# Optimization experiments

Hardware: AMD Instinct MI355X
Metric: run time of the kernel (lower is better)

The kernel has to match this reference:

```python
import jax, jax.numpy as jnp
import numpy as np

N, E = 100_000, 1_000_000
D_IN, D_H, D_OUT = 64, 64, 16


def _lin_init(key, d_in, d_out):
    # torch.nn.Linear default: U(-1/sqrt(fan_in), 1/sqrt(fan_in))
    s = 1.0 / np.sqrt(d_in)
    kw, kb = jax.random.split(key)
    W = jax.random.uniform(kw, (d_in, d_out), jnp.float32, -s, s)
    b = jax.random.uniform(kb, (d_out,), jnp.float32, -s, s)
    return W, b


def setup_inputs() -> dict:
    key = jax.random.key(0)
    ks = jax.random.split(key, 8)
    x = jax.random.normal(ks[0], (N, D_IN), dtype=jnp.float32)
    edge_index = jax.random.randint(ks[1], (2, E), 0, N, dtype=jnp.int64)
    inp = {"x": x, "edge_index": edge_index}
    dims = [(D_IN, D_H), (D_H, D_H), (D_H, D_H), (D_H, D_H)]
    for i, (di, do) in enumerate(dims):
        W, b = _lin_init(ks[2 + i], di, do)
        inp[f"W{i}"] = W
        inp[f"b{i}"] = b
    W_out, b_out = _lin_init(ks[6], D_H, D_OUT)
    inp["W_out"] = W_out
    inp["b_out"] = b_out
    return inp


def gcn_conv(x, W, b, src, dst, deg_inv_sqrt):
    # GCNConv: x' = D^{-1/2} (A + I) D^{-1/2} (x W) + b
    h = x @ W  # [N, D]
    norm = deg_inv_sqrt[src] * deg_inv_sqrt[dst]  # [E]
    msgs = h[src] * norm[:, None]  # gather + scale
    agg = jax.ops.segment_sum(msgs, dst, num_segments=x.shape[0])
    # self-loop contribution: deg^{-1} * h_i
    agg = agg + h * (deg_inv_sqrt * deg_inv_sqrt)[:, None]
    return agg + b


def reference(x, edge_index, W0, b0, W1, b1, W2, b2, W3, b3, W_out, b_out):
    src, dst = edge_index[0], edge_index[1]
    n = x.shape[0]
    # degree over A + I (unit edge weights + self loops), counted at dst (col)
    deg = jax.ops.segment_sum(jnp.ones((src.shape[0],), x.dtype), dst,
                              num_segments=n) + 1.0
    deg_inv_sqrt = jax.lax.rsqrt(deg)

    h = jnp.tanh(gcn_conv(x, W0, b0, src, dst, deg_inv_sqrt))
    h = jnp.tanh(gcn_conv(h, W1, b1, src, dst, deg_inv_sqrt))
    h = jnp.tanh(gcn_conv(h, W2, b2, src, dst, deg_inv_sqrt))
    h = jnp.tanh(gcn_conv(h, W3, b3, src, dst, deg_inv_sqrt))
    return h @ W_out + b_out
```

## Files before the change

### kernel.cpp

```cpp
#include <hip/hip_runtime.h>
#include <hip/hip_bf16.h>
#include <math.h>


#define NBSHIFT 9

typedef __attribute__((ext_vector_type(8))) short short8;
typedef __attribute__((ext_vector_type(4))) float f32x4;

__device__ __forceinline__ float tanh_fast(float x) {
    float e = __expf(2.0f * x);
    return 1.0f - 2.0f / (e + 1.0f);
}
__device__ __forceinline__ unsigned short f2bf(float f) {
    unsigned u = __float_as_uint(f);
    return (unsigned short)((u + 0x7fff + ((u >> 16) & 1)) >> 16);
}
__device__ __forceinline__ float bf2f(unsigned short h) {
    return __uint_as_float((unsigned)h << 16);
}

__global__ void __launch_bounds__(256) deg_kernel(const int* __restrict__ dst,
                                                  int* __restrict__ deg, int E) {
    int i = blockIdx.x * 256 + threadIdx.x;
    if (i < E) atomicAdd(&deg[dst[i]], 1);
}

__global__ void __launch_bounds__(256) dis_kernel(const int* __restrict__ deg,
                                                  float* __restrict__ dis, int n) {
    int i = blockIdx.x * 256 + threadIdx.x;
    if (i < n) dis[i] = rsqrtf((float)deg[i] + 1.0f);
}

__global__ void __launch_bounds__(1024) scan1_kernel(const int* __restrict__ in,
                                                     int* __restrict__ out,
                                                     int* __restrict__ csum, int n) {
    __shared__ int s[1024];
    int t = threadIdx.x;
    int i = blockIdx.x * 1024 + t;
    int v = (i < n) ? in[i] : 0;
    s[t] = v;
    __syncthreads();
    #pragma unroll
    for (int o = 1; o < 1024; o <<= 1) {
        int a = 0;
        if (t >= o) a = s[t - o];
        __syncthreads();
        if (t >= o) s[t] += a;
        __syncthreads();
    }
    if (i < n) out[i] = s[t] - v;
    if (t == 1023) csum[blockIdx.x] = s[1023];
}

__global__ void __launch_bounds__(1024) scan2_kernel(int* __restrict__ csum, int nc) {
    __shared__ int s[1024];
    int t = threadIdx.x;
    int v = (t < nc) ? csum[t] : 0;
    s[t] = v;
    __syncthreads();
    #pragma unroll
    for (int o = 1; o < 1024; o <<= 1) {
        int a = 0;
        if (t >= o) a = s[t - o];
        __syncthreads();
        if (t >= o) s[t] += a;
        __syncthreads();
    }
    if (t < nc) csum[t] = s[t] - v;
}

__global__ void __launch_bounds__(1024) scan3_kernel(int* __restrict__ out,
                                                     const int* __restrict__ csum,
                                                     int n, int total) {
    int i = blockIdx.x * 1024 + threadIdx.x;
    if (i < n) out[i] += csum[blockIdx.x];
    if (i == 0) out[n] = total;
}

__global__ void __launch_bounds__(256) hist_kernel(const int* __restrict__ dst,
                                                   int* __restrict__ hist,
                                                   int E, int NB, int nblocks) {
    __shared__ int lh[256];
    int t = threadIdx.x;
    lh[t] = 0;
    __syncthreads();
    int base = blockIdx.x * 4096;
    int end = base + 4096; if (end > E) end = E;
    for (int i = base + t; i < end; i += 256)
        atomicAdd(&lh[dst[i] >> NBSHIFT], 1);
    __syncthreads();
    if (t < NB) hist[t * nblocks + blockIdx.x] = lh[t];
}

__global__ void __launch_bounds__(256) part_kernel(const int* __restrict__ src,
                                                   const int* __restrict__ dst,
                                                   const int* __restrict__ phist,
                                                   unsigned long long* __restrict__ staged,
                                                   int E, int NB, int nblocks) {
    __shared__ int lcur[256];
    int t = threadIdx.x;
    if (t < NB) lcur[t] = phist[t * nblocks + blockIdx.x];
    __syncthreads();
    int base = blockIdx.x * 4096;
    int end = base + 4096; if (end > E) end = E;
    for (int i = base + t; i < end; i += 256) {
        int d = dst[i];
        int b = d >> NBSHIFT;
        int pos = atomicAdd(&lcur[b], 1);
        staged[pos] = ((unsigned long long)(unsigned)d << 32) | (unsigned)src[i];
    }
}

__global__ void __launch_bounds__(256) fill2_kernel(const unsigned long long* __restrict__ staged,
                                                    const int* __restrict__ phist,
                                                    const int* __restrict__ off,
                                                    int* __restrict__ cursor,
                                                    int* __restrict__ srcl,
                                                    int nblocks) {
    int b = blockIdx.x;
    int r0 = phist[b * nblocks];
    int r1 = phist[(b + 1) * nblocks];
    for (int i = r0 + threadIdx.x; i < r1; i += 256) {
        unsigned long long rec = staged[i];
        int d = (int)(rec >> 32);
        int s = (int)(rec & 0xffffffffu);
        int pos = atomicAdd(&cursor[d], 1);
        srcl[off[d] + pos] = s;
    }
}

__global__ void __launch_bounds__(256) wprep_kernel(const float* __restrict__ W0,
                                                    const float* __restrict__ W1,
                                                    const float* __restrict__ W2,
                                                    const float* __restrict__ W3,
                                                    short* __restrict__ wf) {
    const float* Ws[4] = {W0, W1, W2, W3};
    int l = blockIdx.x;
    const float* Wg = Ws[l];
    int t = threadIdx.x;
    int lane = t & 63;
    int ct = t >> 6;
    #pragma unroll
    for (int kk = 0; kk < 2; ++kk) {
        #pragma unroll
        for (int e = 0; e < 8; ++e) {
            int k = kk * 32 + (lane >> 4) * 8 + e;
            int c = ct * 16 + (lane & 15);
            float w = Wg[k * 64 + c];
            unsigned short hi = f2bf(w);
            unsigned short lo = f2bf(w - bf2f(hi));
            size_t b = ((size_t)l * 4 + ct) * 2 + kk;
            wf[((b * 2 + 0) * 64 + lane) * 8 + e] = (short)hi;
            wf[((b * 2 + 1) * 64 + lane) * 8 + e] = (short)lo;
        }
    }
}

#define SPLIT8(vA, vB, H, L) { \
    float _f[8] = {vA.x, vA.y, vA.z, vA.w, vB.x, vB.y, vB.z, vB.w}; \
    _Pragma("unroll") \
    for (int _e = 0; _e < 8; ++_e) { \
        unsigned short _h = f2bf(_f[_e]); \
        H[_e] = (short)_h; \
        L[_e] = (short)f2bf(_f[_e] - bf2f(_h)); \
    } }

__global__ void __launch_bounds__(256) gemm2_kernel(const float* __restrict__ in,
                                                    const short* __restrict__ wf,
                                                    const float* __restrict__ dis,
                                                    float* __restrict__ g, int n) {
    int t = threadIdx.x;
    int lane = t & 63;
    int wave = t >> 6;
    int c = lane & 15;
    int g4 = lane >> 4;

    short8 Bh[4][2], Bl[4][2];
    #pragma unroll
    for (int ct = 0; ct < 4; ++ct) {
        #pragma unroll
        for (int kk = 0; kk < 2; ++kk) {
            int b = (ct * 2 + kk) * 2;
            Bh[ct][kk] = *(const short8*)(wf + ((size_t)(b + 0) * 64 + lane) * 8);
            Bl[ct][kk] = *(const short8*)(wf + ((size_t)(b + 1) * 64 + lane) * 8);
        }
    }

    int tile = blockIdx.x * 4 + wave;
    int base = tile * 16;
    if (base >= n) return;

    const float4* ap = (const float4*)(in + (size_t)(base + c) * 64 + g4 * 8);
    float4 v00 = ap[0], v01 = ap[1];
    float4 v10 = ap[8], v11 = ap[9];

    short8 Ah0, Al0, Ah1, Al1;
    SPLIT8(v00, v01, Ah0, Al0);
    SPLIT8(v10, v11, Ah1, Al1);

    f32x4 acc[4];
    #pragma unroll
    for (int ct = 0; ct < 4; ++ct) {
        f32x4 a = {0.f, 0.f, 0.f, 0.f};
        a = __builtin_amdgcn_mfma_f32_16x16x32_bf16(Ah0, Bh[ct][0], a, 0, 0, 0);
        a = __builtin_amdgcn_mfma_f32_16x16x32_bf16(Ah1, Bh[ct][1], a, 0, 0, 0);
        a = __builtin_amdgcn_mfma_f32_16x16x32_bf16(Al0, Bh[ct][0], a, 0, 0, 0);
        a = __builtin_amdgcn_mfma_f32_16x16x32_bf16(Al1, Bh[ct][1], a, 0, 0, 0);
        a = __builtin_amdgcn_mfma_f32_16x16x32_bf16(Ah0, Bl[ct][0], a, 0, 0, 0);
        a = __builtin_amdgcn_mfma_f32_16x16x32_bf16(Ah1, Bl[ct][1], a, 0, 0, 0);
        acc[ct] = a;
    }

    f32x4 dvv = *(const f32x4*)(dis + base + g4 * 4);
    #pragma unroll
    for (int ct = 0; ct < 4; ++ct) {
        #pragma unroll
        for (int r = 0; r < 4; ++r) {
            g[(size_t)(base + g4 * 4 + r) * 64 + ct * 16 + c] = dvv[r] * acc[ct][r];
        }
    }
}

__global__ void __launch_bounds__(256) agg_kernel(const float* __restrict__ g,
                                                  const float* __restrict__ dis,
                                                  const int* __restrict__ off,
                                                  const int* __restrict__ srcl,
                                                  const float* __restrict__ bias,
                                                  float* __restrict__ out, int n) {
    int t = threadIdx.x;
    int lane = t & 63;
    int q = lane >> 4;
    int r = lane & 15;
    int node = (blockIdx.x << 4) + ((t >> 6) << 2) + q;
    if (node >= n) return;

    const float4* gv = (const float4*)g;
    float4 s = gv[node * 16 + r];
    int e = off[node], e1 = off[node + 1];
    while (e1 - e >= 8) {
        int i0 = srcl[e + 0], i1 = srcl[e + 1], i2 = srcl[e + 2], i3 = srcl[e + 3];
        int i4 = srcl[e + 4], i5 = srcl[e + 5], i6 = srcl[e + 6], i7 = srcl[e + 7];
        float4 a0 = gv[i0 * 16 + r], a1 = gv[i1 * 16 + r];
        float4 a2 = gv[i2 * 16 + r], a3 = gv[i3 * 16 + r];
        float4 a4 = gv[i4 * 16 + r], a5 = gv[i5 * 16 + r];
        float4 a6 = gv[i6 * 16 + r], a7 = gv[i7 * 16 + r];
        s.x += ((a0.x + a1.x) + (a2.x + a3.x)) + ((a4.x + a5.x) + (a6.x + a7.x));
        s.y += ((a0.y + a1.y) + (a2.y + a3.y)) + ((a4.y + a5.y) + (a6.y + a7.y));
        s.z += ((a0.z + a1.z) + (a2.z + a3.z)) + ((a4.z + a5.z) + (a6.z + a7.z));
        s.w += ((a0.w + a1.w) + (a2.w + a3.w)) + ((a4.w + a5.w) + (a6.w + a7.w));
        e += 8;
    }
    if (e1 - e >= 4) {
        int i0 = srcl[e + 0], i1 = srcl[e + 1], i2 = srcl[e + 2], i3 = srcl[e + 3];
        float4 a0 = gv[i0 * 16 + r], a1 = gv[i1 * 16 + r];
        float4 a2 = gv[i2 * 16 + r], a3 = gv[i3 * 16 + r];
        s.x += (a0.x + a1.x) + (a2.x + a3.x);
        s.y += (a0.y + a1.y) + (a2.y + a3.y);
        s.z += (a0.z + a1.z) + (a2.z + a3.z);
        s.w += (a0.w + a1.w) + (a2.w + a3.w);
        e += 4;
    }
    while (e < e1) {
        float4 a = gv[srcl[e] * 16 + r];
        s.x += a.x; s.y += a.y; s.z += a.z; s.w += a.w;
        ++e;
    }
    float dn = dis[node];
    float4 b = ((const float4*)bias)[r];
    float4 h;
    h.x = tanh_fast(fmaf(dn, s.x, b.x));
    h.y = tanh_fast(fmaf(dn, s.y, b.y));
    h.z = tanh_fast(fmaf(dn, s.z, b.z));
    h.w = tanh_fast(fmaf(dn, s.w, b.w));
    ((float4*)out)[node * 16 + r] = h;
}

__global__ void __launch_bounds__(256) final_kernel(const float* __restrict__ h,
                                                    const float* __restrict__ Wo,
                                                    const float* __restrict__ bo,
                                                    float* __restrict__ out, int n) {
    __shared__ float Wl[1024];
    __shared__ float bl[16];
    __shared__ float hs[16 * 68];
    int t = threadIdx.x;
    for (int i = t; i < 1024; i += 256) Wl[i] = Wo[i];
    if (t < 16) bl[t] = bo[t];
    int nodeBase = blockIdx.x * 16;
    for (int i = t; i < 1024; i += 256) {
        int nn = i >> 6, kk = i & 63;
        if (nodeBase + nn < n) hs[nn * 68 + kk] = h[(nodeBase + nn) * 64 + kk];
    }
    __syncthreads();
    int nsub = t >> 4;
    int j = t & 15;
    int node = nodeBase + nsub;
    if (node >= n) return;
    const float* hr = hs + nsub * 68;
    float acc = bl[j];
    #pragma unroll
    for (int k = 0; k < 64; ++k) acc = fmaf(hr[k], Wl[k * 16 + j], acc);
    out[node * 16 + j] = acc;
}

extern "C" void kernel_launch(void* const* d_in, const int* in_sizes, int n_in,
                              void* d_out, int out_size, void* d_ws, size_t ws_size,
                              hipStream_t stream) {
    const float* x     = (const float*)d_in[0];
    const int*   ei    = (const int*)d_in[1];
    const float* W[4]  = {(const float*)d_in[2], (const float*)d_in[4],
                          (const float*)d_in[6], (const float*)d_in[8]};
    const float* B[4]  = {(const float*)d_in[3], (const float*)d_in[5],
                          (const float*)d_in[7], (const float*)d_in[9]};
    const float* Wo    = (const float*)d_in[10];
    const float* bo    = (const float*)d_in[11];
    float* out         = (float*)d_out;

    const int N = in_sizes[0] / 64;
    const int E = in_sizes[1] / 2;
    const int* srcp = ei;
    const int* dstp = ei + E;

    const int NB       = (N + (1 << NBSHIFT) - 1) >> NBSHIFT;
    const int nblocksP = (E + 4095) / 4096;
    const int NH       = NB * nblocksP;

    char* w = (char*)d_ws;
    size_t o = 0;
    auto alloc = [&](size_t bytes) { void* p = w + o; o = (o + bytes + 255) & ~(size_t)255; return p; };
    float* dis    = (float*)alloc((size_t)N * 4);
    int*   degi   = (int*)  alloc((size_t)N * 4);
    int*   off    = (int*)  alloc((size_t)(N + 1) * 4);
    int*   cursor = (int*)  alloc((size_t)N * 4);
    int*   csum   = (int*)  alloc(4096);
    int*   srcl   = (int*)  alloc((size_t)E * 4);
    int*   hist   = (int*)  alloc((size_t)NH * 4);
    int*   phist  = (int*)  alloc((size_t)(NH + 1) * 4);
    short* wf     = (short*)alloc((size_t)4 * 8192 * 2);
    float* bufA   = (float*)alloc((size_t)N * 64 * 4);
    float* bufB   = (float*)alloc((size_t)N * 64 * 4);
    unsigned long long* staged = (unsigned long long*)bufA;

    hipMemsetAsync(degi,   0, (size_t)N * 4, stream);
    hipMemsetAsync(cursor, 0, (size_t)N * 4, stream);

    int ge   = (E + 255) / 256;
    int gn   = (N + 255) / 256;
    int nchN = (N + 1023) / 1024;
    int nchH = (NH + 1023) / 1024;

    wprep_kernel<<<4, 256, 0, stream>>>(W[0], W[1], W[2], W[3], wf);
    deg_kernel<<<ge, 256, 0, stream>>>(dstp, degi, E);
    dis_kernel<<<gn, 256, 0, stream>>>(degi, dis, N);
    scan1_kernel<<<nchN, 1024, 0, stream>>>(degi, off, csum, N);
    scan2_kernel<<<1, 1024, 0, stream>>>(csum, nchN);
    scan3_kernel<<<nchN, 1024, 0, stream>>>(off, csum, N, E);
    hist_kernel<<<nblocksP, 256, 0, stream>>>(dstp, hist, E, NB, nblocksP);
    scan1_kernel<<<nchH, 1024, 0, stream>>>(hist, phist, csum, NH);
    scan2_kernel<<<1, 1024, 0, stream>>>(csum, nchH);
    scan3_kernel<<<nchH, 1024, 0, stream>>>(phist, csum, NH, E);
    part_kernel<<<nblocksP, 256, 0, stream>>>(srcp, dstp, phist, staged, E, NB, nblocksP);
    fill2_kernel<<<NB, 256, 0, stream>>>(staged, phist, off, cursor, srcl, nblocksP);

    int tiles     = (N + 15) / 16;
    int g2_blocks = (tiles + 3) / 4;
    int agg_blocks = (N + 15) / 16;

    const float* cur = x;
    for (int l = 0; l < 4; ++l) {
        gemm2_kernel<<<g2_blocks, 256, 0, stream>>>(cur, wf + (size_t)l * 8192, dis, bufA, N);
        agg_kernel<<<agg_blocks, 256, 0, stream>>>(bufA, dis, off, srcl, B[l], bufB, N);
        cur = bufB;
    }
    final_kernel<<<(N + 15) / 16, 256, 0, stream>>>(bufB, Wo, bo, out, N);
}
```

Before: 426.0 us.

## Fuse aggregation with next-layer GEMM and derive degrees from bucketed edges

```diff
diff --git a/kernel.cpp b/kernel.cpp
--- a/kernel.cpp
+++ b/kernel.cpp
@@ -18,18 +18,6 @@
 }
 __device__ __forceinline__ float bf2f(unsigned short h) {
     return __uint_as_float((unsigned)h << 16);
-}
-
-__global__ void __launch_bounds__(256) deg_kernel(const int* __restrict__ dst,
-                                                  int* __restrict__ deg, int E) {
-    int i = blockIdx.x * 256 + threadIdx.x;
-    if (i < E) atomicAdd(&deg[dst[i]], 1);
-}
-
-__global__ void __launch_bounds__(256) dis_kernel(const int* __restrict__ deg,
-                                                  float* __restrict__ dis, int n) {
-    int i = blockIdx.x * 256 + threadIdx.x;
-    if (i < n) dis[i] = rsqrtf((float)deg[i] + 1.0f);
 }
 
 __global__ void __launch_bounds__(1024) scan1_kernel(const int* __restrict__ in,
@@ -96,7 +84,7 @@
 __global__ void __launch_bounds__(256) part_kernel(const int* __restrict__ src,
                                                    const int* __restrict__ dst,
                                                    const int* __restrict__ phist,
-                                                   unsigned long long* __restrict__ staged,
+                                                   unsigned* __restrict__ staged,
                                                    int E, int NB, int nblocks) {
     __shared__ int lcur[256];
     int t = threadIdx.x;
@@ -108,25 +96,56 @@
         int d = dst[i];
         int b = d >> NBSHIFT;
         int pos = atomicAdd(&lcur[b], 1);
-        staged[pos] = ((unsigned long long)(unsigned)d << 32) | (unsigned)src[i];
-    }
-}
-
-__global__ void __launch_bounds__(256) fill2_kernel(const unsigned long long* __restrict__ staged,
+        staged[pos] = ((unsigned)(d & 511) << 17) | (unsigned)src[i];
+    }
+}
+
+__global__ void __launch_bounds__(256) bdeg_kernel(const unsigned* __restrict__ staged,
+                                                   const int* __restrict__ phist,
+                                                   int* __restrict__ deg,
+                                                   float* __restrict__ dis,
+                                                   int nblocks, int n) {
+    __shared__ int ldeg[512];
+    int b = blockIdx.x, t = threadIdx.x;
+    ldeg[t] = 0; ldeg[t + 256] = 0;
+    __syncthreads();
+    int r0 = phist[b * nblocks];
+    int r1 = phist[(b + 1) * nblocks];
+    for (int i = r0 + t; i < r1; i += 256)
+        atomicAdd(&ldeg[staged[i] >> 17], 1);
+    __syncthreads();
+    int gbase = b << NBSHIFT;
+    #pragma unroll
+    for (int k = 0; k < 2; ++k) {
+        int li = t + k * 256, gi = gbase + li;
+        if (gi < n) {
+            int d = ldeg[li];
+            deg[gi] = d;
+            dis[gi] = rsqrtf((float)d + 1.0f);
+        }
+    }
+}
+
+__global__ void __launch_bounds__(256) fill3_kernel(const unsigned* __restrict__ staged,
                                                     const int* __restrict__ phist,
                                                     const int* __restrict__ off,
-                                                    int* __restrict__ cursor,
                                                     int* __restrict__ srcl,
-                                                    int nblocks) {
-    int b = blockIdx.x;
+                                                    int nblocks, int n) {
+    __shared__ int lcur[512];
+    int b = blockIdx.x, t = threadIdx.x;
+    int gbase = b << NBSHIFT;
+    #pragma unroll
+    for (int k = 0; k < 2; ++k) {
+        int li = t + k * 256, gi = gbase + li;
+        lcur[li] = (gi < n) ? off[gi] : 0;
+    }
+    __syncthreads();
     int r0 = phist[b * nblocks];
     int r1 = phist[(b + 1) * nblocks];
-    for (int i = r0 + threadIdx.x; i < r1; i += 256) {
-        unsigned long long rec = staged[i];
-        int d = (int)(rec >> 32);
-        int s = (int)(rec & 0xffffffffu);
-        int pos = atomicAdd(&cursor[d], 1);
-        srcl[off[d] + pos] = s;
+    for (int i = r0 + t; i < r1; i += 256) {
+        unsigned rec = staged[i];
+        int pos = atomicAdd(&lcur[rec >> 17], 1);
+        srcl[pos] = (int)(rec & 0x1FFFFu);
     }
 }
 
@@ -166,78 +185,9 @@
         L[_e] = (short)f2bf(_f[_e] - bf2f(_h)); \
     } }
 
-__global__ void __launch_bounds__(256) gemm2_kernel(const float* __restrict__ in,
-                                                    const short* __restrict__ wf,
-                                                    const float* __restrict__ dis,
-                                                    float* __restrict__ g, int n) {
-    int t = threadIdx.x;
-    int lane = t & 63;
-    int wave = t >> 6;
-    int c = lane & 15;
-    int g4 = lane >> 4;
-
-    short8 Bh[4][2], Bl[4][2];
-    #pragma unroll
-    for (int ct = 0; ct < 4; ++ct) {
-        #pragma unroll
-        for (int kk = 0; kk < 2; ++kk) {
-            int b = (ct * 2 + kk) * 2;
-            Bh[ct][kk] = *(const short8*)(wf + ((size_t)(b + 0) * 64 + lane) * 8);
-            Bl[ct][kk] = *(const short8*)(wf + ((size_t)(b + 1) * 64 + lane) * 8);
-        }
-    }
-
-    int tile = blockIdx.x * 4 + wave;
-    int base = tile * 16;
-    if (base >= n) return;
-
-    const float4* ap = (const float4*)(in + (size_t)(base + c) * 64 + g4 * 8);
-    float4 v00 = ap[0], v01 = ap[1];
-    float4 v10 = ap[8], v11 = ap[9];
-
-    short8 Ah0, Al0, Ah1, Al1;
-    SPLIT8(v00, v01, Ah0, Al0);
-    SPLIT8(v10, v11, Ah1, Al1);
-
-    f32x4 acc[4];
-    #pragma unroll
-    for (int ct = 0; ct < 4; ++ct) {
-        f32x4 a = {0.f, 0.f, 0.f, 0.f};
-        a = __builtin_amdgcn_mfma_f32_16x16x32_bf16(Ah0, Bh[ct][0], a, 0, 0, 0);
-        a = __builtin_amdgcn_mfma_f32_16x16x32_bf16(Ah1, Bh[ct][1], a, 0, 0, 0);
-        a = __builtin_amdgcn_mfma_f32_16x16x32_bf16(Al0, Bh[ct][0], a, 0, 0, 0);
-        a = __builtin_amdgcn_mfma_f32_16x16x32_bf16(Al1, Bh[ct][1], a, 0, 0, 0);
-        a = __builtin_amdgcn_mfma_f32_16x16x32_bf16(Ah0, Bl[ct][0], a, 0, 0, 0);
-        a = __builtin_amdgcn_mfma_f32_16x16x32_bf16(Ah1, Bl[ct][1], a, 0, 0, 0);
-        acc[ct] = a;
-    }
-
-    f32x4 dvv = *(const f32x4*)(dis + base + g4 * 4);
-    #pragma unroll
-    for (int ct = 0; ct < 4; ++ct) {
-        #pragma unroll
-        for (int r = 0; r < 4; ++r) {
-            g[(size_t)(base + g4 * 4 + r) * 64 + ct * 16 + c] = dvv[r] * acc[ct][r];
-        }
-    }
-}
-
-__global__ void __launch_bounds__(256) agg_kernel(const float* __restrict__ g,
-                                                  const float* __restrict__ dis,
-                                                  const int* __restrict__ off,
-                                                  const int* __restrict__ srcl,
-                                                  const float* __restrict__ bias,
-                                                  float* __restrict__ out, int n) {
-    int t = threadIdx.x;
-    int lane = t & 63;
-    int q = lane >> 4;
-    int r = lane & 15;
-    int node = (blockIdx.x << 4) + ((t >> 6) << 2) + q;
-    if (node >= n) return;
-
-    const float4* gv = (const float4*)g;
-    float4 s = gv[node * 16 + r];
-    int e = off[node], e1 = off[node + 1];
+__device__ __forceinline__ float4 gather_row(const float4* __restrict__ gv,
+                                             const int* __restrict__ srcl,
+                                             int e, int e1, float4 s, int r) {
     while (e1 - e >= 8) {
         int i0 = srcl[e + 0], i1 = srcl[e + 1], i2 = srcl[e + 2], i3 = srcl[e + 3];
         int i4 = srcl[e + 4], i5 = srcl[e + 5], i6 = srcl[e + 6], i7 = srcl[e + 7];
@@ -266,41 +216,198 @@
         s.x += a.x; s.y += a.y; s.z += a.z; s.w += a.w;
         ++e;
     }
-    float dn = dis[node];
-    float4 b = ((const float4*)bias)[r];
-    float4 h;
-    h.x = tanh_fast(fmaf(dn, s.x, b.x));
-    h.y = tanh_fast(fmaf(dn, s.y, b.y));
-    h.z = tanh_fast(fmaf(dn, s.z, b.z));
-    h.w = tanh_fast(fmaf(dn, s.w, b.w));
-    ((float4*)out)[node * 16 + r] = h;
-}
-
-__global__ void __launch_bounds__(256) final_kernel(const float* __restrict__ h,
-                                                    const float* __restrict__ Wo,
-                                                    const float* __restrict__ bo,
-                                                    float* __restrict__ out, int n) {
+    return s;
+}
+
+__global__ void __launch_bounds__(256) gemm2_kernel(const float* __restrict__ in,
+                                                    const short* __restrict__ wf,
+                                                    const float* __restrict__ dis,
+                                                    float* __restrict__ g, int n) {
+    int t = threadIdx.x;
+    int lane = t & 63;
+    int wave = t >> 6;
+    int c = lane & 15;
+    int g4 = lane >> 4;
+
+    short8 Bh[4][2], Bl[4][2];
+    #pragma unroll
+    for (int ct = 0; ct < 4; ++ct) {
+        #pragma unroll
+        for (int kk = 0; kk < 2; ++kk) {
+            int b = (ct * 2 + kk) * 2;
+            Bh[ct][kk] = *(const short8*)(wf + ((size_t)(b + 0) * 64 + lane) * 8);
+            Bl[ct][kk] = *(const short8*)(wf + ((size_t)(b + 1) * 64 + lane) * 8);
+        }
+    }
+
+    int tile = blockIdx.x * 4 + wave;
+    int base = tile * 16;
+    if (base >= n) return;
+
+    const float4* ap = (const float4*)(in + (size_t)(base + c) * 64 + g4 * 8);
+    float4 v00 = ap[0], v01 = ap[1];
+    float4 v10 = ap[8], v11 = ap[9];
+
+    short8 Ah0, Al0, Ah1, Al1;
+    SPLIT8(v00, v01, Ah0, Al0);
+    SPLIT8(v10, v11, Ah1, Al1);
+
+    f32x4 acc[4];
+    #pragma unroll
+    for (int ct = 0; ct < 4; ++ct) {
+        f32x4 a = {0.f, 0.f, 0.f, 0.f};
+        a = __builtin_amdgcn_mfma_f32_16x16x32_bf16(Ah0, Bh[ct][0], a, 0, 0, 0);
+        a = __builtin_amdgcn_mfma_f32_16x16x32_bf16(Ah1, Bh[ct][1], a, 0, 0, 0);
+        a = __builtin_amdgcn_mfma_f32_16x16x32_bf16(Al0, Bh[ct][0], a, 0, 0, 0);
+        a = __builtin_amdgcn_mfma_f32_16x16x32_bf16(Al1, Bh[ct][1], a, 0, 0, 0);
+        a = __builtin_amdgcn_mfma_f32_16x16x32_bf16(Ah0, Bl[ct][0], a, 0, 0, 0);
+        a = __builtin_amdgcn_mfma_f32_16x16x32_bf16(Ah1, Bl[ct][1], a, 0, 0, 0);
+        acc[ct] = a;
+    }
+
+    f32x4 dvv = *(const f32x4*)(dis + base + g4 * 4);
+    #pragma unroll
+    for (int ct = 0; ct < 4; ++ct) {
+        #pragma unroll
+        for (int r = 0; r < 4; ++r) {
+            g[(size_t)(base + g4 * 4 + r) * 64 + ct * 16 + c] = dvv[r] * acc[ct][r];
+        }
+    }
+}
+
+__global__ void __launch_bounds__(256) fused_kernel(const float* __restrict__ g_in,
+                                                    const float* __restrict__ dis,
+                                                    const int* __restrict__ off,
+                                                    const int* __restrict__ srcl,
+                                                    const float* __restrict__ bias,
+                                                    const short* __restrict__ wfn,
+                                                    float* __restrict__ g_out, int n) {
+    __shared__ float hs[64][68];
+    int t = threadIdx.x;
+    int base = blockIdx.x * 64;
+    int r = t & 15;
+    int qq = t >> 4;
+    const float4* gv = (const float4*)g_in;
+    float4 b4 = ((const float4*)bias)[r];
+
+    #pragma unroll
+    for (int p = 0; p < 4; ++p) {
+        int nl = p * 16 + qq;
+        int node = base + nl;
+        if (node < n) {
+            float4 s = gv[(size_t)node * 16 + r];
+            float4 sg = gather_row(gv, srcl, off[node], off[node + 1], s, r);
+            float dn = dis[node];
+            hs[nl][r * 4 + 0] = tanh_fast(fmaf(dn, sg.x, b4.x));
+            hs[nl][r * 4 + 1] = tanh_fast(fmaf(dn, sg.y, b4.y));
+            hs[nl][r * 4 + 2] = tanh_fast(fmaf(dn, sg.z, b4.z));
+            hs[nl][r * 4 + 3] = tanh_fast(fmaf(dn, sg.w, b4.w));
+        }
+    }
+    __syncthreads();
+
+    int lane = t & 63;
+    int wave = t >> 6;
+    int c = lane & 15;
+    int g4 = lane >> 4;
+    int obase = base + wave * 16;
+    if (obase >= n) return;
+
+    short8 Bh[4][2], Bl[4][2];
+    #pragma unroll
+    for (int ct = 0; ct < 4; ++ct) {
+        #pragma unroll
+        for (int kk = 0; kk < 2; ++kk) {
+            int b = (ct * 2 + kk) * 2;
+            Bh[ct][kk] = *(const short8*)(wfn + ((size_t)(b + 0) * 64 + lane) * 8);
+            Bl[ct][kk] = *(const short8*)(wfn + ((size_t)(b + 1) * 64 + lane) * 8);
+        }
+    }
+
+    const float* hr = &hs[wave * 16 + c][0];
+    float4 v00 = *(const float4*)(hr + g4 * 8);
+    float4 v01 = *(const float4*)(hr + g4 * 8 + 4);
+    float4 v10 = *(const float4*)(hr + g4 * 8 + 32);
+    float4 v11 = *(const float4*)(hr + g4 * 8 + 36);
+
+    short8 Ah0, Al0, Ah1, Al1;
+    SPLIT8(v00, v01, Ah0, Al0);
+    SPLIT8(v10, v11, Ah1, Al1);
+
+    f32x4 acc[4];
+    #pragma unroll
+    for (int ct = 0; ct < 4; ++ct) {
+        f32x4 a = {0.f, 0.f, 0.f, 0.f};
+        a = __builtin_amdgcn_mfma_f32_16x16x32_bf16(Ah0, Bh[ct][0], a, 0, 0, 0);
+        a = __builtin_amdgcn_mfma_f32_16x16x32_bf16(Ah1, Bh[ct][1], a, 0, 0, 0);
+        a = __builtin_amdgcn_mfma_f32_16x16x32_bf16(Al0, Bh[ct][0], a, 0, 0, 0);
+        a = __builtin_amdgcn_mfma_f32_16x16x32_bf16(Al1, Bh[ct][1], a, 0, 0, 0);
+        a = __builtin_amdgcn_mfma_f32_16x16x32_bf16(Ah0, Bl[ct][0], a, 0, 0, 0);
+        a = __builtin_amdgcn_mfma_f32_16x16x32_bf16(Ah1, Bl[ct][1], a, 0, 0, 0);
+        acc[ct] = a;
+    }
+
+    f32x4 dvv = *(const f32x4*)(dis + obase + g4 * 4);
+    #pragma unroll
+    for (int ct = 0; ct < 4; ++ct) {
+        #pragma unroll
+        for (int rr = 0; rr < 4; ++rr) {
+            g_out[(size_t)(obase + g4 * 4 + rr) * 64 + ct * 16 + c] = dvv[rr] * acc[ct][rr];
+        }
+    }
+}
+
+__global__ void __launch_bounds__(256) fused_final_kernel(const float* __restrict__ g_in,
+                                                          const float* __restrict__ dis,
+                                                          const int* __restrict__ off,
+                                                          const int* __restrict__ srcl,
+                                                          const float* __restrict__ bias,
+                                                          const float* __restrict__ Wo,
+                                                          const float* __restrict__ bo,
+                                                          float* __restrict__ out, int n) {
+    __shared__ float hs[64][68];
     __shared__ float Wl[1024];
     __shared__ float bl[16];
-    __shared__ float hs[16 * 68];
     int t = threadIdx.x;
     for (int i = t; i < 1024; i += 256) Wl[i] = Wo[i];
     if (t < 16) bl[t] = bo[t];
-    int nodeBase = blockIdx.x * 16;
-    for (int i = t; i < 1024; i += 256) {
-        int nn = i >> 6, kk = i & 63;
-        if (nodeBase + nn < n) hs[nn * 68 + kk] = h[(nodeBase + nn) * 64 + kk];
-    }
-    __syncthreads();
+
+    int base = blockIdx.x * 64;
+    int r = t & 15;
+    int qq = t >> 4;
+    const float4* gv = (const float4*)g_in;
+    float4 b4 = ((const float4*)bias)[r];
+
+    #pragma unroll
+    for (int p = 0; p < 4; ++p) {
+        int nl = p * 16 + qq;
+        int node = base + nl;
+        if (node < n) {
+            float4 s = gv[(size_t)node * 16 + r];
+            float4 sg = gather_row(gv, srcl, off[node], off[node + 1], s, r);
+            float dn = dis[node];
+            hs[nl][r * 4 + 0] = tanh_fast(fmaf(dn, sg.x, b4.x));
+            hs[nl][r * 4 + 1] = tanh_fast(fmaf(dn, sg.y, b4.y));
+            hs[nl][r * 4 + 2] = tanh_fast(fmaf(dn, sg.z, b4.z));
+            hs[nl][r * 4 + 3] = tanh_fast(fmaf(dn, sg.w, b4.w));
+        }
+    }
+    __syncthreads();
+
     int nsub = t >> 4;
     int j = t & 15;
-    int node = nodeBase + nsub;
-    if (node >= n) return;
-    const float* hr = hs + nsub * 68;
-    float acc = bl[j];
-    #pragma unroll
-    for (int k = 0; k < 64; ++k) acc = fmaf(hr[k], Wl[k * 16 + j], acc);
-    out[node * 16 + j] = acc;
+    #pragma unroll
+    for (int p = 0; p < 4; ++p) {
+        int nl = p * 16 + nsub;
+        int node = base + nl;
+        if (node < n) {
+            const float* hr = &hs[nl][0];
+            float acc = bl[j];
+            #pragma unroll
+            for (int k = 0; k < 64; ++k) acc = fmaf(hr[k], Wl[k * 16 + j], acc);
+            out[(size_t)node * 16 + j] = acc;
+        }
+    }
 }
 
 extern "C" void kernel_launch(void* const* d_in, const int* in_sizes, int n_in,
@@ -328,49 +435,44 @@
     char* w = (char*)d_ws;
     size_t o = 0;
     auto alloc = [&](size_t bytes) { void* p = w + o; o = (o + bytes + 255) & ~(size_t)255; return p; };
-    float* dis    = (float*)alloc((size_t)N * 4);
-    int*   degi   = (int*)  alloc((size_t)N * 4);
-    int*   off    = (int*)  alloc((size_t)(N + 1) * 4);
-    int*   cursor = (int*)  alloc((size_t)N * 4);
-    int*   csum   = (int*)  alloc(4096);
-    int*   srcl   = (int*)  alloc((size_t)E * 4);
-    int*   hist   = (int*)  alloc((size_t)NH * 4);
-    int*   phist  = (int*)  alloc((size_t)(NH + 1) * 4);
-    short* wf     = (short*)alloc((size_t)4 * 8192 * 2);
-    float* bufA   = (float*)alloc((size_t)N * 64 * 4);
-    float* bufB   = (float*)alloc((size_t)N * 64 * 4);
-    unsigned long long* staged = (unsigned long long*)bufA;
-
-    hipMemsetAsync(degi,   0, (size_t)N * 4, stream);
-    hipMemsetAsync(cursor, 0, (size_t)N * 4, stream);
-
-    int ge   = (E + 255) / 256;
-    int gn   = (N + 255) / 256;
+    float*    dis    = (float*)alloc((size_t)N * 4);
+    int*      degi   = (int*)  alloc((size_t)N * 4);
+    int*      off    = (int*)  alloc((size_t)(N + 1) * 4);
+    int*      csum   = (int*)  alloc(4096);
+    int*      srcl   = (int*)  alloc((size_t)E * 4);
+    int*      hist   = (int*)  alloc((size_t)NH * 4);
+    int*      phist  = (int*)  alloc((size_t)(NH + 1) * 4);
+    short*    wf     = (short*)alloc((size_t)4 * 8192 * 2);
+    float*    bufA   = (float*)alloc((size_t)N * 64 * 4);
+    float*    bufB   = (float*)alloc((size_t)N * 64 * 4);
+    unsigned* staged = (unsigned*)bufA;
+
     int nchN = (N + 1023) / 1024;
     int nchH = (NH + 1023) / 1024;
 
     wprep_kernel<<<4, 256, 0, stream>>>(W[0], W[1], W[2], W[3], wf);
-    deg_kernel<<<ge, 256, 0, stream>>>(dstp, degi, E);
-    dis_kernel<<<gn, 256, 0, stream>>>(degi, dis, N);
-    scan1_kernel<<<nchN, 1024, 0, stream>>>(degi, off, csum, N);
-    scan2_kernel<<<1, 1024, 0, stream>>>(csum, nchN);
-    scan3_kernel<<<nchN, 1024, 0, stream>>>(off, csum, N, E);
     hist_kernel<<<nblocksP, 256, 0, stream>>>(dstp, hist, E, NB, nblocksP);
     scan1_kernel<<<nchH, 1024, 0, stream>>>(hist, phist, csum, NH);
     scan2_kernel<<<1, 1024, 0, stream>>>(csum, nchH);
     scan3_kernel<<<nchH, 1024, 0, stream>>>(phist, csum, NH, E);
     part_kernel<<<nblocksP, 256, 0, stream>>>(srcp, dstp, phist, staged, E, NB, nblocksP);
-    fill2_kernel<<<NB, 256, 0, stream>>>(staged, phist, off, cursor, srcl, nblocksP);
+    bdeg_kernel<<<NB, 256, 0, stream>>>(staged, phist, degi, dis, nblocksP, N);
+    scan1_kernel<<<nchN, 1024, 0, stream>>>(degi, off, csum, N);
+    scan2_kernel<<<1, 1024, 0, stream>>>(csum, nchN);
+    scan3_kernel<<<nchN, 1024, 0, stream>>>(off, csum, N, E);
+    fill3_kernel<<<NB, 256, 0, stream>>>(staged, phist, off, srcl, nblocksP, N);
 
     int tiles     = (N + 15) / 16;
     int g2_blocks = (tiles + 3) / 4;
-    int agg_blocks = (N + 15) / 16;
-
-    const float* cur = x;
-    for (int l = 0; l < 4; ++l) {
-        gemm2_kernel<<<g2_blocks, 256, 0, stream>>>(cur, wf + (size_t)l * 8192, dis, bufA, N);
-        agg_kernel<<<agg_blocks, 256, 0, stream>>>(bufA, dis, off, srcl, B[l], bufB, N);
-        cur = bufB;
-    }
-    final_kernel<<<(N + 15) / 16, 256, 0, stream>>>(bufB, Wo, bo, out, N);
-}
+    int f_blocks  = (N + 63) / 64;
+
+    gemm2_kernel<<<g2_blocks, 256, 0, stream>>>(x, wf, dis, bufA, N);
+    fused_kernel<<<f_blocks, 256, 0, stream>>>(bufA, dis, off, srcl, B[0],
+                                               wf + (size_t)1 * 8192, bufB, N);
+    fused_kernel<<<f_blocks, 256, 0, stream>>>(bufB, dis, off, srcl, B[1],
+                                               wf + (size_t)2 * 8192, bufA, N);
+    fused_kernel<<<f_blocks, 256, 0, stream>>>(bufA, dis, off, srcl, B[2],
+                                               wf + (size_t)3 * 8192, bufB, N);
+    fused_final_kernel<<<f_blocks, 256, 0, stream>>>(bufB, dis, off, srcl, B[3],
+                                                     Wo, bo, out, N);
+}
```

After: 367.5 us. -13.7%, faster.
